# Kernel optimization log

Hardware: AMD Instinct MI355X
Metric: run time of the kernel (lower is better)

Reference implementation:

```python
import jax, jax.numpy as jnp
import numpy as np

H = 512        # hidden_size
ENC = 2 * H    # encoder (context) feature dim
V = 10000      # vocab_size
B, T, L = 32, 500, 100
NEG_INF = -1e10


def setup_inputs() -> dict:
    key = jax.random.key(0)
    ks = jax.random.split(key, 16)
    sc = 0.02
    inp = {
        "h_batch": jax.random.normal(ks[0], (B, T, ENC), jnp.float32),
        "seq_lens": jax.random.randint(ks[1], (B,), 1, T + 1),
        "labels": jax.random.randint(ks[2], (B, L), 0, V),
        # content-based (additive) attention params
        "attn_Ws": jax.random.normal(ks[3], (H, H), jnp.float32) * sc,
        "attn_Wh": jax.random.normal(ks[4], (ENC, H), jnp.float32) * sc,
        "attn_b": jnp.zeros((H,), jnp.float32),
        "attn_v": jax.random.normal(ks[5], (H,), jnp.float32) * sc,
        # output path
        "W_sy": jax.random.normal(ks[6], (H, H), jnp.float32) * sc,
        "b_sy": jnp.zeros((H,), jnp.float32),
        "W_gy": jax.random.normal(ks[7], (ENC, H), jnp.float32) * sc,
        "b_gy": jnp.zeros((H,), jnp.float32),
        "W_yy": jax.random.normal(ks[8], (H, V), jnp.float32) * sc,
        "b_yy": jnp.zeros((V,), jnp.float32),
        # recurrence path
        "E_yr": jax.random.normal(ks[9], (V, 4 * H), jnp.float32) * sc,
        "W_sr": jax.random.normal(ks[10], (H, 4 * H), jnp.float32) * sc,
        "b_sr": jnp.zeros((4 * H,), jnp.float32),
        "W_gr": jax.random.normal(ks[11], (ENC, 4 * H), jnp.float32) * sc,
        "b_gr": jnp.zeros((4 * H,), jnp.float32),
    }
    return inp


def _func_lstm(rec_in, c):
    i, f, g, o = jnp.split(rec_in, 4, axis=-1)
    c_new = jax.nn.sigmoid(f) * c + jax.nn.sigmoid(i) * jnp.tanh(g)
    s_new = jax.nn.sigmoid(o) * jnp.tanh(c_new)
    return s_new, c_new


def reference(h_batch, seq_lens, labels, attn_Ws, attn_Wh, attn_b, attn_v,
              W_sy, b_sy, W_gy, b_gy, W_yy, b_yy,
              E_yr, W_sr, b_sr, W_gr, b_gr):
    Tlen = h_batch.shape[1]
    mask = jnp.arange(Tlen)[None, :] < seq_lens[:, None]          # [B,T]
    h_proj = jnp.einsum('bte,eh->bth', h_batch, attn_Wh) + attn_b  # precompute

    s0 = jnp.zeros((h_batch.shape[0], H), h_batch.dtype)
    c0 = jnp.zeros_like(s0)

    def step(carry, y_t):
        s, c = carry
        # content-based attention: e = v . tanh(Ws s + Wh h)
        e = jnp.einsum('bth,h->bt', jnp.tanh(h_proj + (s @ attn_Ws)[:, None, :]), attn_v)
        e = jnp.where(mask, e, NEG_INF)
        alpha = jax.nn.softmax(e, axis=-1)                         # [B,T]
        g = jnp.einsum('bt,bte->be', alpha, h_batch)               # [B,ENC]
        dec_feat = (g @ W_gy + b_gy) + (s @ W_sy + b_sy)
        y = jnp.tanh(dec_feat) @ W_yy + b_yy                       # [B,V]
        rec_in = E_yr[y_t] + (s @ W_sr + b_sr) + (g @ W_gr + b_gr) # [B,4H]
        s_new, c_new = _func_lstm(rec_in, c)
        return (s_new, c_new), y

    _, preds = jax.lax.scan(step, (s0, c0), labels.T)              # [L,B,V]
    return jnp.transpose(preds, (1, 0, 2))                         # [B,L,V]
```

## Files before the change

kernel.cpp:

```cpp
#include <hip/hip_runtime.h>
#include <cstdint>

#define B_   32
#define T_   500
#define H_   512
#define ENC_ 1024
#define V_   10000
#define L_   100
#define H4_  2048
#define NB_  256
#define NT_  512

#define OFF_HPROJ 0
#define OFF_WYYP  4096000
#define OFF_WRECP 9216000
#define OFF_WSB   13148160
#define OFF_S     13279232
#define OFF_C0    13295616
#define OFF_C1    13312000
#define OFF_RACC  13328384
#define OFF_DACC  13393920
#define OFF_G0    13410304
#define OFF_G1    13443072
#define OFF_E     13475840
#define OFF_BAR   13492224
#define ZERO_CNT  213056

using bf16x8 = __attribute__((ext_vector_type(8))) short;
using f32x4  = __attribute__((ext_vector_type(4))) float;

__device__ __forceinline__ f32x4 mfma16(bf16x8 a, bf16x8 b, f32x4 c){
  return __builtin_amdgcn_mfma_f32_16x16x32_bf16(a, b, c, 0, 0, 0);
}
__device__ __forceinline__ unsigned short bfr(float f){
  unsigned x = __float_as_uint(f);
  return (unsigned short)((x + 0x7FFFu + ((x>>16)&1u)) >> 16);
}
__device__ __forceinline__ void bfsplit(float f, short& hi, short& lo){
  unsigned short h = bfr(f);
  float hf = __uint_as_float(((unsigned)h) << 16);
  hi = (short)h;
  lo = (short)bfr(f - hf);
}
__device__ __forceinline__ float bf2f(unsigned short u){
  return __uint_as_float(((unsigned)u) << 16);
}
__device__ __forceinline__ float ftanh(float x){
  float t = fminf(fmaxf(2.f*x, -30.f), 30.f);
  float e = __expf(t);
  return (e - 1.f) / (e + 1.f);
}
__device__ __forceinline__ float fsig(float x){
  float t = fminf(fmaxf(x, -30.f), 30.f);
  return 1.f / (1.f + __expf(-t));
}
__device__ __forceinline__ float gload(const float* p){
  return __hip_atomic_load((float*)p, __ATOMIC_RELAXED, __HIP_MEMORY_SCOPE_AGENT);
}
__device__ __forceinline__ void gstore(float* p, float v){
  __hip_atomic_store(p, v, __ATOMIC_RELAXED, __HIP_MEMORY_SCOPE_AGENT);
}
__device__ __forceinline__ void gload2(const float* p, float& a, float& b){
  unsigned long long u = __hip_atomic_load((const unsigned long long*)p,
                          __ATOMIC_RELAXED, __HIP_MEMORY_SCOPE_AGENT);
  a = __uint_as_float((unsigned)u);
  b = __uint_as_float((unsigned)(u >> 32));
}

__device__ __forceinline__ void gridbar(unsigned* bars, unsigned it){
  asm volatile("s_waitcnt vmcnt(0) lgkmcnt(0)" ::: "memory");
  __syncthreads();
  if (threadIdx.x == 0){
    unsigned* gc = bars + 1 + (blockIdx.x & 15);
    unsigned old = __hip_atomic_fetch_add(gc, 1u, __ATOMIC_RELAXED, __HIP_MEMORY_SCOPE_AGENT);
    if (old == it*16u + 15u)
      __hip_atomic_fetch_add(bars, 1u, __ATOMIC_RELAXED, __HIP_MEMORY_SCOPE_AGENT);
    while (__hip_atomic_load(bars, __ATOMIC_RELAXED, __HIP_MEMORY_SCOPE_AGENT) < (it+1u)*16u)
      __builtin_amdgcn_s_sleep(2);
  }
  __syncthreads();
  asm volatile("" ::: "memory");
}

__global__ void k_init(float* __restrict__ ws){
  int i = blockIdx.x * 256 + threadIdx.x;
  if (i < ZERO_CNT) ws[OFF_S + i] = 0.f;
}

__global__ void k_packWyy(const float* __restrict__ Wyy, float* __restrict__ ws){
  unsigned short* wp = (unsigned short*)(ws + OFF_WYYP);
  int t = blockIdx.x * 256 + threadIdx.x;
  if (t >= 625*16*64) return;
  int vt = t / 1024;
  int rem = t - vt*1024;
  int kc = rem >> 6, lane = rem & 63;
  int v  = vt*16 + (lane & 15);
  int k0 = kc*32 + ((lane >> 4) << 3);
  bf16x8 H, Lo;
  #pragma unroll
  for (int j = 0; j < 8; ++j){
    short h, lo; bfsplit(Wyy[(size_t)(k0+j)*V_ + v], h, lo);
    H[j] = h; Lo[j] = lo;
  }
  size_t base = ((size_t)(vt*16 + kc)*2)*512 + (size_t)lane*8;
  *(bf16x8*)(wp + base) = H;
  *(bf16x8*)(wp + base + 512) = Lo;
}

__global__ void k_packWrec(const float* __restrict__ Wsy, const float* __restrict__ Wgy,
                           const float* __restrict__ Wsr, const float* __restrict__ Wgr,
                           float* __restrict__ ws){
  unsigned short* wp = (unsigned short*)(ws + OFF_WRECP);
  int t = blockIdx.x * 256 + threadIdx.x;
  if (t >= 160*48*64) return;
  int vt = t / (48*64);
  int rem = t - vt*(48*64);
  int kc = rem >> 6, lane = rem & 63;
  int col = vt*16 + (lane & 15);
  int k0  = kc*32 + ((lane >> 4) << 3);
  bf16x8 H, Lo;
  #pragma unroll
  for (int j = 0; j < 8; ++j){
    int k = k0 + j;
    float x;
    if (k < 512) x = (col < 512) ? Wsy[(size_t)k*512 + col] : Wsr[(size_t)k*2048 + (col-512)];
    else         x = (col < 512) ? Wgy[(size_t)(k-512)*512 + col] : Wgr[(size_t)(k-512)*2048 + (col-512)];
    short h, lo; bfsplit(x, h, lo);
    H[j] = h; Lo[j] = lo;
  }
  size_t base = ((size_t)(vt*48 + kc)*2)*512 + (size_t)lane*8;
  *(bf16x8*)(wp + base) = H;
  *(bf16x8*)(wp + base + 512) = Lo;
}

__global__ void k_packWs(const float* __restrict__ Ws, float* __restrict__ ws){
  unsigned short* wp = (unsigned short*)(ws + OFF_WSB);
  int i = blockIdx.x * 256 + threadIdx.x;
  wp[i] = bfr(Ws[i]);
}

__global__ void k_hproj(const float* __restrict__ A, const float* __restrict__ W,
                        const float* __restrict__ bias, const int* __restrict__ lens,
                        float* __restrict__ ws){
  unsigned short* C = (unsigned short*)(ws + OFF_HPROJ);
  const int bm = blockIdx.x * 64;
  const int bn = blockIdx.y * 64;
  {
    int b0 = bm / T_, t0 = bm % T_;
    int b1 = (bm + 63) / T_;
    if (b0 == b1 && t0 >= lens[b0]) return;
  }
  __shared__ float As[64][33];
  __shared__ float Bs[32][68];
  const int tid = threadIdx.x;
  const int tx = tid & 15, ty = tid >> 4;
  float acc[4][4];
  #pragma unroll
  for (int i = 0; i < 4; ++i)
    #pragma unroll
    for (int j = 0; j < 4; ++j) acc[i][j] = 0.f;
  for (int k0 = 0; k0 < 1024; k0 += 32){
    for (int i = tid; i < 64*32; i += 256){
      int rr = i >> 5, cc = i & 31;
      As[rr][cc] = A[(size_t)(bm + rr) * 1024 + k0 + cc];
    }
    for (int i = tid; i < 32*64; i += 256){
      int rr = i >> 6, cc = i & 63;
      Bs[rr][cc] = W[(size_t)(k0 + rr) * 512 + bn + cc];
    }
    __syncthreads();
    #pragma unroll
    for (int kk = 0; kk < 32; ++kk){
      float a0 = As[ty*4+0][kk], a1 = As[ty*4+1][kk];
      float a2 = As[ty*4+2][kk], a3 = As[ty*4+3][kk];
      float4 b4 = *(const float4*)&Bs[kk][tx*4];
      acc[0][0] += a0*b4.x; acc[0][1] += a0*b4.y; acc[0][2] += a0*b4.z; acc[0][3] += a0*b4.w;
      acc[1][0] += a1*b4.x; acc[1][1] += a1*b4.y; acc[1][2] += a1*b4.z; acc[1][3] += a1*b4.w;
      acc[2][0] += a2*b4.x; acc[2][1] += a2*b4.y; acc[2][2] += a2*b4.z; acc[2][3] += a2*b4.w;
      acc[3][0] += a3*b4.x; acc[3][1] += a3*b4.y; acc[3][2] += a3*b4.z; acc[3][3] += a3*b4.w;
    }
    __syncthreads();
  }
  #pragma unroll
  for (int i = 0; i < 4; ++i){
    int m = bm + ty*4 + i;
    ushort4 o;
    o.x = bfr(acc[i][0] + bias[bn + tx*4 + 0]);
    o.y = bfr(acc[i][1] + bias[bn + tx*4 + 1]);
    o.z = bfr(acc[i][2] + bias[bn + tx*4 + 2]);
    o.w = bfr(acc[i][3] + bias[bn + tx*4 + 3]);
    *(ushort4*)&C[(size_t)m * 512 + bn + tx*4] = o;
  }
}

__global__ __launch_bounds__(NT_, 2) void k_persist(
    const float* __restrict__ hb,  const int* __restrict__ lens,
    const int* __restrict__ labels, const float* __restrict__ av,
    const float* __restrict__ bsy, const float* __restrict__ bgy,
    const float* __restrict__ byy,
    const float* __restrict__ Eyr,
    const float* __restrict__ bsr, const float* __restrict__ bgr,
    float* __restrict__ out, float* __restrict__ ws)
{
  const int blk = blockIdx.x;
  const int tid = threadIdx.x;
  const int w   = tid >> 6;
  const int lane= tid & 63;
  unsigned* bars = (unsigned*)(ws + OFF_BAR);
  const unsigned short* wyyp  = (const unsigned short*)(ws + OFF_WYYP);
  const unsigned short* wrecp = (const unsigned short*)(ws + OFF_WRECP);
  const unsigned short* wsb   = (const unsigned short*)(ws + OFF_WSB);
  const unsigned short* hpB   = (const unsigned short*)(ws + OFF_HPROJ);
  __shared__ __align__(16) float smem[4096];

  const int arow  = lane & 15;
  const int klane = (lane >> 4) << 3;
  float c_reg = 0.f;

  for (int l = 0; l <= L_; ++l){
    const int p = l & 1;
    const int goff = p ? OFF_G1 : OFF_G0;
    if (blk < 157){
      if (l > 0){
        const int kh = w & 1;
        const int vtslot = w >> 1;
        const int vt = blk*4 + vtslot;
        f32x4 a0 = {0.f,0.f,0.f,0.f}, a1 = {0.f,0.f,0.f,0.f};
        if (vt < 625){
          for (int kc2 = 0; kc2 < 8; ++kc2){
            const int kc = kh*8 + kc2;
            const int k0 = kc*32 + klane;
            float bb[8];
            {
              float4 y1 = *(const float4*)&bsy[k0];
              float4 y2 = *(const float4*)&bsy[k0+4];
              float4 y3 = *(const float4*)&bgy[k0];
              float4 y4 = *(const float4*)&bgy[k0+4];
              bb[0]=y1.x+y3.x; bb[1]=y1.y+y3.y; bb[2]=y1.z+y3.z; bb[3]=y1.w+y3.w;
              bb[4]=y2.x+y4.x; bb[5]=y2.y+y4.y; bb[6]=y2.z+y4.z; bb[7]=y2.w+y4.w;
            }
            bf16x8 Ahi0, Alo0, Ahi1, Alo1;
            {
              float x[8];
              gload2(&ws[OFF_DACC + arow*H_ + k0 + 0], x[0], x[1]);
              gload2(&ws[OFF_DACC + arow*H_ + k0 + 2], x[2], x[3]);
              gload2(&ws[OFF_DACC + arow*H_ + k0 + 4], x[4], x[5]);
              gload2(&ws[OFF_DACC + arow*H_ + k0 + 6], x[6], x[7]);
              #pragma unroll
              for (int j = 0; j < 8; ++j){
                short h, lo; bfsplit(ftanh(x[j] + bb[j]), h, lo);
                Ahi0[j] = h; Alo0[j] = lo;
              }
            }
            {
              float x[8];
              gload2(&ws[OFF_DACC + (arow+16)*H_ + k0 + 0], x[0], x[1]);
              gload2(&ws[OFF_DACC + (arow+16)*H_ + k0 + 2], x[2], x[3]);
              gload2(&ws[OFF_DACC + (arow+16)*H_ + k0 + 4], x[4], x[5]);
              gload2(&ws[OFF_DACC + (arow+16)*H_ + k0 + 6], x[6], x[7]);
              #pragma unroll
              for (int j = 0; j < 8; ++j){
                short h, lo; bfsplit(ftanh(x[j] + bb[j]), h, lo);
                Ahi1[j] = h; Alo1[j] = lo;
              }
            }
            const unsigned short* wp = wyyp + ((size_t)(vt*16 + kc)*2)*512 + (size_t)lane*8;
            bf16x8 Bhi = *(const bf16x8*)wp;
            bf16x8 Blo = *(const bf16x8*)(wp + 512);
            a0 = mfma16(Ahi0, Bhi, a0);
            a0 = mfma16(Alo0, Bhi, a0);
            a0 = mfma16(Ahi0, Blo, a0);
            a1 = mfma16(Ahi1, Bhi, a1);
            a1 = mfma16(Alo1, Bhi, a1);
            a1 = mfma16(Ahi1, Blo, a1);
          }
        }
        if (vt < 625 && kh == 0){
          #pragma unroll
          for (int r = 0; r < 4; ++r){
            smem[vtslot*512 +       lane*4 + r] = a0[r];
            smem[vtslot*512 + 256 + lane*4 + r] = a1[r];
          }
        }
        __syncthreads();
        if (vt < 625 && kh == 1){
          const int v = vt*16 + arow;
          const float bv = byy[v];
          const int lv = l - 1;
          #pragma unroll
          for (int r = 0; r < 4; ++r){
            const int row0 = ((lane >> 4) << 2) + r;
            float v0 = smem[vtslot*512 +       lane*4 + r] + a0[r] + bv;
            float v1 = smem[vtslot*512 + 256 + lane*4 + r] + a1[r] + bv;
            out[((size_t)(row0)*L_      + lv)*V_ + v] = v0;
            out[((size_t)(row0 + 16)*L_ + lv)*V_ + v] = v1;
          }
        }
        __syncthreads();
      }
    } else if (blk < 221){
      if (l < L_){
        const int u = blk - 157;
        const int b = u >> 1, half = u & 1;
        float* ssm = smem;
        float* part = smem + 512;
        float* wsm = smem + 2560;
        if (l == 0){
          ssm[tid] = 0.f;
          c_reg = 0.f;
        } else {
          const int h = tid;
          const float* ey = Eyr + (size_t)labels[b*L_ + (l-1)] * H4_;
          float ri = gload(&ws[OFF_RACC + b*H4_ + h])        + bsr[h]      + bgr[h]      + ey[h];
          float rf = gload(&ws[OFF_RACC + b*H4_ + 512 + h])  + bsr[512+h]  + bgr[512+h]  + ey[512+h];
          float rg = gload(&ws[OFF_RACC + b*H4_ + 1024 + h]) + bsr[1024+h] + bgr[1024+h] + ey[1024+h];
          float ro = gload(&ws[OFF_RACC + b*H4_ + 1536 + h]) + bsr[1536+h] + bgr[1536+h] + ey[1536+h];
          float cn = fsig(rf)*c_reg + fsig(ri)*ftanh(rg);
          float sn = fsig(ro)*ftanh(cn);
          c_reg = cn;
          if (half == 0) gstore(&ws[OFF_S + b*H_ + h], sn);
          ssm[h] = sn;
        }
        __syncthreads();
        {
          const int colp = tid & 255;
          const int kh2  = tid >> 8;
          const int col0 = colp*2;
          const float* sp = ssm + kh2*256;
          const unsigned short* wb = wsb + (size_t)(kh2*256)*512 + col0;
          float acc0 = 0.f, acc1 = 0.f;
          for (int k = 0; k < 256; k += 8){
            float4 s0 = *(const float4*)&sp[k];
            float4 s1 = *(const float4*)&sp[k+4];
            unsigned wv[8];
            #pragma unroll
            for (int j = 0; j < 8; ++j)
              wv[j] = *(const unsigned*)&wb[(size_t)(k+j)*512];
            float sv[8] = {s0.x,s0.y,s0.z,s0.w,s1.x,s1.y,s1.z,s1.w};
            #pragma unroll
            for (int j = 0; j < 8; ++j){
              acc0 += sv[j] * bf2f((unsigned short)(wv[j] & 0xFFFFu));
              acc1 += sv[j] * bf2f((unsigned short)(wv[j] >> 16));
            }
          }
          part[kh2*1024 + col0]     = acc0;
          part[kh2*1024 + col0 + 1] = acc1;
        }
        __syncthreads();
        wsm[tid] = part[tid] + part[1024 + tid];
        __syncthreads();
        const int len = lens[b];
        float avr[8], swr[8];
        #pragma unroll
        for (int j = 0; j < 8; ++j){
          avr[j] = av[lane*8 + j];
          swr[j] = wsm[lane*8 + j];
        }
        float* e = ws + OFF_E;
        for (int t = 2*w + half; t < len; t += 16){
          bf16x8 hp = *(const bf16x8*)&hpB[(size_t)(b*T_ + t)*512 + lane*8];
          float sum = 0.f;
          #pragma unroll
          for (int j = 0; j < 8; ++j)
            sum += avr[j] * ftanh(bf2f((unsigned short)hp[j]) + swr[j]);
          #pragma unroll
          for (int off = 32; off > 0; off >>= 1) sum += __shfl_xor(sum, off, 64);
          if (lane == 0) gstore(&e[b*T_ + t], sum);
        }
      }
    } else {
      if (l < L_){
        for (int i = (blk - 221)*NT_ + tid; i < B_*ENC_; i += 35*NT_)
          gstore(&ws[goff + i], 0.f);
      }
    }
    if (l == L_) break;
    gridbar(bars, (unsigned)(l*3 + 0));

    {
      const int b = blk >> 3, ts = blk & 7;
      const int len = lens[b];
      float* sc  = smem;
      float* red = smem + 512;
      float* pg  = smem + 1024;
      float val = (tid < len) ? gload(&ws[OFF_E + b*T_ + tid]) : -1e30f;
      sc[tid] = val;
      __syncthreads();
      if (tid < 256) red[tid] = fmaxf(sc[tid], sc[tid+256]);
      __syncthreads();
      for (int st = 128; st > 0; st >>= 1){
        if (tid < st) red[tid] = fmaxf(red[tid], red[tid+st]);
        __syncthreads();
      }
      const float mx = red[0];
      __syncthreads();
      float ex = (tid < len) ? __expf(val - mx) : 0.f;
      sc[tid] = ex;
      __syncthreads();
      if (tid < 256) red[tid] = sc[tid] + sc[tid+256];
      __syncthreads();
      for (int st = 128; st > 0; st >>= 1){
        if (tid < st) red[tid] += red[tid+st];
        __syncthreads();
      }
      const float inv = 1.f / red[0];
      const int tg  = tid >> 8;
      const int cq  = tid & 255;
      const int col = cq * 4;
      const float* hp = hb + (size_t)b*T_*ENC_ + col;
      float4 acc = {0.f,0.f,0.f,0.f};
      for (int t = ts*2 + tg; t < len; t += 16){
        float4 x = *(const float4*)&hp[(size_t)t * ENC_];
        float a = sc[t];
        acc.x += a*x.x; acc.y += a*x.y; acc.z += a*x.z; acc.w += a*x.w;
      }
      *(float4*)&pg[tg*1024 + col] = acc;
      __syncthreads();
      if (tid < 256){
        float4 x0 = *(const float4*)&pg[col];
        float4 x1 = *(const float4*)&pg[1024 + col];
        float* gp = ws + goff + b*ENC_ + col;
        atomicAdd(gp+0, (x0.x+x1.x)*inv);
        atomicAdd(gp+1, (x0.y+x1.y)*inv);
        atomicAdd(gp+2, (x0.z+x1.z)*inv);
        atomicAdd(gp+3, (x0.w+x1.w)*inv);
      }
    }
    gridbar(bars, (unsigned)(l*3 + 1));

    if (blk < 80){
      const int sub = w >> 2;
      const int w4  = w & 3;
      const int vt  = blk*2 + sub;
      f32x4 acc0 = {0.f,0.f,0.f,0.f}, acc1 = {0.f,0.f,0.f,0.f};
      for (int c = 0; c < 3; ++c){
        #pragma unroll
        for (int kc2 = 0; kc2 < 4; ++kc2){
          const int kc = c*16 + w4*4 + kc2;
          const int k0 = kc*32 + klane;
          bf16x8 Ahi0, Alo0, Ahi1, Alo1;
          {
            const float* src = (k0 < 512) ? &ws[OFF_S + arow*H_ + k0]
                                          : &ws[goff + arow*ENC_ + (k0 - 512)];
            float x[8];
            gload2(src+0, x[0], x[1]);
            gload2(src+2, x[2], x[3]);
            gload2(src+4, x[4], x[5]);
            gload2(src+6, x[6], x[7]);
            #pragma unroll
            for (int j = 0; j < 8; ++j){
              short h, lo; bfsplit(x[j], h, lo);
              Ahi0[j] = h; Alo0[j] = lo;
            }
          }
          {
            const float* src = (k0 < 512) ? &ws[OFF_S + (arow+16)*H_ + k0]
                                          : &ws[goff + (arow+16)*ENC_ + (k0 - 512)];
            float x[8];
            gload2(src+0, x[0], x[1]);
            gload2(src+2, x[2], x[3]);
            gload2(src+4, x[4], x[5]);
            gload2(src+6, x[6], x[7]);
            #pragma unroll
            for (int j = 0; j < 8; ++j){
              short h, lo; bfsplit(x[j], h, lo);
              Ahi1[j] = h; Alo1[j] = lo;
            }
          }
          const unsigned short* wp = wrecp + ((size_t)(vt*48 + kc)*2)*512 + (size_t)lane*8;
          bf16x8 Bhi = *(const bf16x8*)wp;
          bf16x8 Blo = *(const bf16x8*)(wp + 512);
          acc0 = mfma16(Ahi0, Bhi, acc0);
          acc0 = mfma16(Alo0, Bhi, acc0);
          acc0 = mfma16(Ahi0, Blo, acc0);
          acc1 = mfma16(Ahi1, Bhi, acc1);
          acc1 = mfma16(Alo1, Bhi, acc1);
          acc1 = mfma16(Ahi1, Blo, acc1);
        }
      }
      #pragma unroll
      for (int r = 0; r < 4; ++r){
        smem[sub*2048 + w4*512 +       lane*4 + r] = acc0[r];
        smem[sub*2048 + w4*512 + 256 + lane*4 + r] = acc1[r];
      }
      __syncthreads();
      #pragma unroll
      for (int oo = 0; oo < 2; ++oo){
        const int q   = tid + oo*512;
        const int sb  = q >> 9;
        const int rem = q & 511;
        const int bt  = rem >> 8;
        const int r8  = rem & 255;
        const int ln  = r8 >> 2, rr = r8 & 3;
        float v = smem[sb*2048 +        bt*256 + r8] + smem[sb*2048 +  512 + bt*256 + r8]
                + smem[sb*2048 + 1024 + bt*256 + r8] + smem[sb*2048 + 1536 + bt*256 + r8];
        const int row = bt*16 + ((ln >> 4) << 2) + rr;
        const int col = (blk*2 + sb)*16 + (ln & 15);
        if (col < 512) gstore(&ws[OFF_DACC + row*H_ + col], v);
        else           gstore(&ws[OFF_RACC + row*H4_ + (col - 512)], v);
      }
    }
    gridbar(bars, (unsigned)(l*3 + 2));
  }
}

extern "C" void kernel_launch(void* const* d_in, const int* in_sizes, int n_in,
                              void* d_out, int out_size, void* d_ws, size_t ws_size,
                              hipStream_t stream){
  const float* h_batch = (const float*)d_in[0];
  const int*   seq_lens= (const int*)d_in[1];
  const int*   labels  = (const int*)d_in[2];
  const float* attn_Ws = (const float*)d_in[3];
  const float* attn_Wh = (const float*)d_in[4];
  const float* attn_b  = (const float*)d_in[5];
  const float* attn_v  = (const float*)d_in[6];
  const float* W_sy    = (const float*)d_in[7];
  const float* b_sy    = (const float*)d_in[8];
  const float* W_gy    = (const float*)d_in[9];
  const float* b_gy    = (const float*)d_in[10];
  const float* W_yy    = (const float*)d_in[11];
  const float* b_yy    = (const float*)d_in[12];
  const float* E_yr    = (const float*)d_in[13];
  const float* W_sr    = (const float*)d_in[14];
  const float* b_sr    = (const float*)d_in[15];
  const float* W_gr    = (const float*)d_in[16];
  const float* b_gr    = (const float*)d_in[17];
  float* out = (float*)d_out;
  float* ws  = (float*)d_ws;

  k_init    <<<833, 256, 0, stream>>>(ws);
  k_packWyy <<<2500, 256, 0, stream>>>(W_yy, ws);
  k_packWrec<<<1920, 256, 0, stream>>>(W_sy, W_gy, W_sr, W_gr, ws);
  k_packWs  <<<1024, 256, 0, stream>>>(attn_Ws, ws);
  k_hproj   <<<dim3(250, 8), 256, 0, stream>>>(h_batch, attn_Wh, attn_b, seq_lens, ws);

  void* kargs[] = {
    (void*)&h_batch, (void*)&seq_lens, (void*)&labels, (void*)&attn_v,
    (void*)&b_sy, (void*)&b_gy, (void*)&b_yy,
    (void*)&E_yr, (void*)&b_sr, (void*)&b_gr,
    (void*)&out, (void*)&ws
  };
  hipLaunchCooperativeKernel((void*)k_persist, dim3(NB_), dim3(NT_), kargs, 0, stream);
}
```

Before: 10.82 ms.

## Use 1024-thread persistent blocks and bf16 copy of encoder states

Doubles the block size of the persistent cooperative kernel to 1024 threads with one block per CU. Work is redistributed so fewer blocks handle the vocab projection and recurrence GEMMs, and more waves handle attention scoring. A pre-pass converts h_batch to bf16 so the context-vector reduction reads half the bytes. Partial sums are now combined with shared-memory atomics, and the count of cross-block atomics on g drops. The trade-off is fewer resident waves per CU, an extra conversion kernel over 16M elements, and bf16 rounding of the encoder states in the context sum.

```diff
diff --git a/kernel.cpp b/kernel.cpp
--- a/kernel.cpp
+++ b/kernel.cpp
@@ -9,22 +9,21 @@
 #define L_   100
 #define H4_  2048
 #define NB_  256
-#define NT_  512
+#define NT_  1024
 
 #define OFF_HPROJ 0
 #define OFF_WYYP  4096000
 #define OFF_WRECP 9216000
 #define OFF_WSB   13148160
-#define OFF_S     13279232
-#define OFF_C0    13295616
-#define OFF_C1    13312000
-#define OFF_RACC  13328384
-#define OFF_DACC  13393920
-#define OFF_G0    13410304
-#define OFF_G1    13443072
-#define OFF_E     13475840
-#define OFF_BAR   13492224
-#define ZERO_CNT  213056
+#define OFF_HB16  13279232
+#define OFF_S     21471232
+#define OFF_RACC  21487616
+#define OFF_DACC  21553152
+#define OFF_G0    21569536
+#define OFF_G1    21602304
+#define OFF_E     21635072
+#define OFF_BAR   21651456
+#define ZERO_CNT  180288
 
 using bf16x8 = __attribute__((ext_vector_type(8))) short;
 using f32x4  = __attribute__((ext_vector_type(4))) float;
@@ -137,6 +136,12 @@
   unsigned short* wp = (unsigned short*)(ws + OFF_WSB);
   int i = blockIdx.x * 256 + threadIdx.x;
   wp[i] = bfr(Ws[i]);
+}
+
+__global__ void k_packHB(const float* __restrict__ hb, float* __restrict__ ws){
+  unsigned short* wp = (unsigned short*)(ws + OFF_HB16);
+  int i = blockIdx.x * 256 + threadIdx.x;
+  if (i < B_*T_*ENC_) wp[i] = bfr(hb[i]);
 }
 
 __global__ void k_hproj(const float* __restrict__ A, const float* __restrict__ W,
@@ -193,8 +198,8 @@
   }
 }
 
-__global__ __launch_bounds__(NT_, 2) void k_persist(
-    const float* __restrict__ hb,  const int* __restrict__ lens,
+__global__ __launch_bounds__(NT_, 1) void k_persist(
+    const int* __restrict__ lens,
     const int* __restrict__ labels, const float* __restrict__ av,
     const float* __restrict__ bsy, const float* __restrict__ bgy,
     const float* __restrict__ byy,
@@ -211,7 +216,8 @@
   const unsigned short* wrecp = (const unsigned short*)(ws + OFF_WRECP);
   const unsigned short* wsb   = (const unsigned short*)(ws + OFF_WSB);
   const unsigned short* hpB   = (const unsigned short*)(ws + OFF_HPROJ);
-  __shared__ __align__(16) float smem[4096];
+  const unsigned short* hb16  = (const unsigned short*)(ws + OFF_HB16);
+  __shared__ __align__(16) float smem[10240];
 
   const int arow  = lane & 15;
   const int klane = (lane >> 4) << 3;
@@ -220,13 +226,16 @@
   for (int l = 0; l <= L_; ++l){
     const int p = l & 1;
     const int goff = p ? OFF_G1 : OFF_G0;
-    if (blk < 157){
+    if (blk < 79){
       if (l > 0){
+        const int vtslot = w >> 1;
         const int kh = w & 1;
-        const int vtslot = w >> 1;
-        const int vt = blk*4 + vtslot;
-        f32x4 a0 = {0.f,0.f,0.f,0.f}, a1 = {0.f,0.f,0.f,0.f};
+        const int vt = blk*8 + vtslot;
+        float* cacc = smem;
+        for (int i = tid; i < 4096; i += NT_) cacc[i] = 0.f;
+        __syncthreads();
         if (vt < 625){
+          f32x4 a0 = {0.f,0.f,0.f,0.f}, a1 = {0.f,0.f,0.f,0.f};
           for (int kc2 = 0; kc2 < 8; ++kc2){
             const int kc = kh*8 + kc2;
             const int k0 = kc*32 + klane;
@@ -274,62 +283,60 @@
             a1 = mfma16(Alo1, Bhi, a1);
             a1 = mfma16(Ahi1, Blo, a1);
           }
-        }
-        if (vt < 625 && kh == 0){
           #pragma unroll
           for (int r = 0; r < 4; ++r){
-            smem[vtslot*512 +       lane*4 + r] = a0[r];
-            smem[vtslot*512 + 256 + lane*4 + r] = a1[r];
-          }
-        }
-        __syncthreads();
-        if (vt < 625 && kh == 1){
-          const int v = vt*16 + arow;
-          const float bv = byy[v];
-          const int lv = l - 1;
-          #pragma unroll
-          for (int r = 0; r < 4; ++r){
-            const int row0 = ((lane >> 4) << 2) + r;
-            float v0 = smem[vtslot*512 +       lane*4 + r] + a0[r] + bv;
-            float v1 = smem[vtslot*512 + 256 + lane*4 + r] + a1[r] + bv;
-            out[((size_t)(row0)*L_      + lv)*V_ + v] = v0;
-            out[((size_t)(row0 + 16)*L_ + lv)*V_ + v] = v1;
-          }
-        }
-        __syncthreads();
-      }
-    } else if (blk < 221){
+            atomicAdd(&cacc[vtslot*512 +       lane*4 + r], a0[r]);
+            atomicAdd(&cacc[vtslot*512 + 256 + lane*4 + r], a1[r]);
+          }
+        }
+        __syncthreads();
+        const int lv = l - 1;
+        #pragma unroll
+        for (int ii = 0; ii < 4; ++ii){
+          const int i = tid + ii*NT_;
+          const int vts = i >> 9, e9 = i & 511;
+          const int vto = blk*8 + vts;
+          if (vto < 625){
+            const int bt = e9 >> 8, r8 = e9 & 255, ln = r8 >> 2, rr = r8 & 3;
+            const int row = bt*16 + ((ln >> 4) << 2) + rr;
+            const int v = vto*16 + (ln & 15);
+            out[((size_t)row*L_ + lv)*V_ + v] = cacc[i] + byy[v];
+          }
+        }
+      }
+    } else if (blk < 207){
       if (l < L_){
-        const int u = blk - 157;
-        const int b = u >> 1, half = u & 1;
-        float* ssm = smem;
+        const int u = blk - 79;
+        const int b = u >> 2, q = u & 3;
+        float* ssm  = smem;
         float* part = smem + 512;
-        float* wsm = smem + 2560;
+        float* wsm  = smem + 2560;
         if (l == 0){
-          ssm[tid] = 0.f;
-          c_reg = 0.f;
+          if (tid < 512){ ssm[tid] = 0.f; c_reg = 0.f; }
         } else {
-          const int h = tid;
-          const float* ey = Eyr + (size_t)labels[b*L_ + (l-1)] * H4_;
-          float ri = gload(&ws[OFF_RACC + b*H4_ + h])        + bsr[h]      + bgr[h]      + ey[h];
-          float rf = gload(&ws[OFF_RACC + b*H4_ + 512 + h])  + bsr[512+h]  + bgr[512+h]  + ey[512+h];
-          float rg = gload(&ws[OFF_RACC + b*H4_ + 1024 + h]) + bsr[1024+h] + bgr[1024+h] + ey[1024+h];
-          float ro = gload(&ws[OFF_RACC + b*H4_ + 1536 + h]) + bsr[1536+h] + bgr[1536+h] + ey[1536+h];
-          float cn = fsig(rf)*c_reg + fsig(ri)*ftanh(rg);
-          float sn = fsig(ro)*ftanh(cn);
-          c_reg = cn;
-          if (half == 0) gstore(&ws[OFF_S + b*H_ + h], sn);
-          ssm[h] = sn;
+          if (tid < 512){
+            const int h = tid;
+            const float* ey = Eyr + (size_t)labels[b*L_ + (l-1)] * H4_;
+            float ri = gload(&ws[OFF_RACC + b*H4_ + h])        + bsr[h]      + bgr[h]      + ey[h];
+            float rf = gload(&ws[OFF_RACC + b*H4_ + 512 + h])  + bsr[512+h]  + bgr[512+h]  + ey[512+h];
+            float rg = gload(&ws[OFF_RACC + b*H4_ + 1024 + h]) + bsr[1024+h] + bgr[1024+h] + ey[1024+h];
+            float ro = gload(&ws[OFF_RACC + b*H4_ + 1536 + h]) + bsr[1536+h] + bgr[1536+h] + ey[1536+h];
+            float cn = fsig(rf)*c_reg + fsig(ri)*ftanh(rg);
+            float sn = fsig(ro)*ftanh(cn);
+            c_reg = cn;
+            if (q == 0) gstore(&ws[OFF_S + b*H_ + h], sn);
+            ssm[h] = sn;
+          }
         }
         __syncthreads();
         {
           const int colp = tid & 255;
-          const int kh2  = tid >> 8;
+          const int ksec = tid >> 8;
           const int col0 = colp*2;
-          const float* sp = ssm + kh2*256;
-          const unsigned short* wb = wsb + (size_t)(kh2*256)*512 + col0;
+          const float* sp = ssm + ksec*128;
+          const unsigned short* wb = wsb + (size_t)(ksec*128)*512 + col0;
           float acc0 = 0.f, acc1 = 0.f;
-          for (int k = 0; k < 256; k += 8){
+          for (int k = 0; k < 128; k += 8){
             float4 s0 = *(const float4*)&sp[k];
             float4 s1 = *(const float4*)&sp[k+4];
             unsigned wv[8];
@@ -343,11 +350,12 @@
               acc1 += sv[j] * bf2f((unsigned short)(wv[j] >> 16));
             }
           }
-          part[kh2*1024 + col0]     = acc0;
-          part[kh2*1024 + col0 + 1] = acc1;
-        }
-        __syncthreads();
-        wsm[tid] = part[tid] + part[1024 + tid];
+          part[ksec*512 + col0]     = acc0;
+          part[ksec*512 + col0 + 1] = acc1;
+        }
+        __syncthreads();
+        if (tid < 512)
+          wsm[tid] = part[tid] + part[512+tid] + part[1024+tid] + part[1536+tid];
         __syncthreads();
         const int len = lens[b];
         float avr[8], swr[8];
@@ -357,7 +365,7 @@
           swr[j] = wsm[lane*8 + j];
         }
         float* e = ws + OFF_E;
-        for (int t = 2*w + half; t < len; t += 16){
+        for (int t = w*4 + q; t < len; t += 64){
           bf16x8 hp = *(const bf16x8*)&hpB[(size_t)(b*T_ + t)*512 + lane*8];
           float sum = 0.f;
           #pragma unroll
@@ -368,9 +376,9 @@
           if (lane == 0) gstore(&e[b*T_ + t], sum);
         }
       }
-    } else {
+    } else if (blk < 223){
       if (l < L_){
-        for (int i = (blk - 221)*NT_ + tid; i < B_*ENC_; i += 35*NT_)
+        for (int i = (blk - 207)*NT_ + tid; i < B_*ENC_; i += 16*NT_)
           gstore(&ws[goff + i], 0.f);
       }
     }
@@ -383,8 +391,10 @@
       float* sc  = smem;
       float* red = smem + 512;
       float* pg  = smem + 1024;
-      float val = (tid < len) ? gload(&ws[OFF_E + b*T_ + tid]) : -1e30f;
-      sc[tid] = val;
+      if (tid < 512){
+        float val = (tid < len) ? gload(&ws[OFF_E + b*T_ + tid]) : -1e30f;
+        sc[tid] = val;
+      }
       __syncthreads();
       if (tid < 256) red[tid] = fmaxf(sc[tid], sc[tid+256]);
       __syncthreads();
@@ -394,8 +404,10 @@
       }
       const float mx = red[0];
       __syncthreads();
-      float ex = (tid < len) ? __expf(val - mx) : 0.f;
-      sc[tid] = ex;
+      if (tid < 512){
+        float ex = (tid < len) ? __expf(sc[tid] - mx) : 0.f;
+        sc[tid] = ex;
+      }
       __syncthreads();
       if (tid < 256) red[tid] = sc[tid] + sc[tid+256];
       __syncthreads();
@@ -404,96 +416,90 @@
         __syncthreads();
       }
       const float inv = 1.f / red[0];
-      const int tg  = tid >> 8;
-      const int cq  = tid & 255;
-      const int col = cq * 4;
-      const float* hp = hb + (size_t)b*T_*ENC_ + col;
-      float4 acc = {0.f,0.f,0.f,0.f};
-      for (int t = ts*2 + tg; t < len; t += 16){
-        float4 x = *(const float4*)&hp[(size_t)t * ENC_];
+      const int tg = tid >> 7;
+      const int cl = tid & 127;
+      const int col0 = cl*8;
+      const unsigned short* hp = hb16 + (size_t)b*T_*ENC_ + col0;
+      float acc[8] = {0.f,0.f,0.f,0.f,0.f,0.f,0.f,0.f};
+      for (int t = ts*8 + tg; t < len; t += 64){
+        bf16x8 x = *(const bf16x8*)&hp[(size_t)t * ENC_];
         float a = sc[t];
-        acc.x += a*x.x; acc.y += a*x.y; acc.z += a*x.z; acc.w += a*x.w;
-      }
-      *(float4*)&pg[tg*1024 + col] = acc;
-      __syncthreads();
-      if (tid < 256){
-        float4 x0 = *(const float4*)&pg[col];
-        float4 x1 = *(const float4*)&pg[1024 + col];
-        float* gp = ws + goff + b*ENC_ + col;
-        atomicAdd(gp+0, (x0.x+x1.x)*inv);
-        atomicAdd(gp+1, (x0.y+x1.y)*inv);
-        atomicAdd(gp+2, (x0.z+x1.z)*inv);
-        atomicAdd(gp+3, (x0.w+x1.w)*inv);
+        #pragma unroll
+        for (int j = 0; j < 8; ++j)
+          acc[j] += a * bf2f((unsigned short)x[j]);
+      }
+      *(float4*)&pg[tg*1024 + col0]     = *(float4*)&acc[0];
+      *(float4*)&pg[tg*1024 + col0 + 4] = *(float4*)&acc[4];
+      __syncthreads();
+      if (ts*8 < len){
+        float s = pg[tid] + pg[1024+tid] + pg[2048+tid] + pg[3072+tid]
+                + pg[4096+tid] + pg[5120+tid] + pg[6144+tid] + pg[7168+tid];
+        atomicAdd(&ws[goff + b*ENC_ + tid], s * inv);
       }
     }
     gridbar(bars, (unsigned)(l*3 + 1));
 
     if (blk < 80){
-      const int sub = w >> 2;
-      const int w4  = w & 3;
+      const int sub = w >> 3;
+      const int w8  = w & 7;
       const int vt  = blk*2 + sub;
+      float* cacc = smem;
+      for (int i = tid; i < 1024; i += NT_) cacc[i] = 0.f;
+      __syncthreads();
       f32x4 acc0 = {0.f,0.f,0.f,0.f}, acc1 = {0.f,0.f,0.f,0.f};
-      for (int c = 0; c < 3; ++c){
-        #pragma unroll
-        for (int kc2 = 0; kc2 < 4; ++kc2){
-          const int kc = c*16 + w4*4 + kc2;
-          const int k0 = kc*32 + klane;
-          bf16x8 Ahi0, Alo0, Ahi1, Alo1;
-          {
-            const float* src = (k0 < 512) ? &ws[OFF_S + arow*H_ + k0]
-                                          : &ws[goff + arow*ENC_ + (k0 - 512)];
-            float x[8];
-            gload2(src+0, x[0], x[1]);
-            gload2(src+2, x[2], x[3]);
-            gload2(src+4, x[4], x[5]);
-            gload2(src+6, x[6], x[7]);
-            #pragma unroll
-            for (int j = 0; j < 8; ++j){
-              short h, lo; bfsplit(x[j], h, lo);
-              Ahi0[j] = h; Alo0[j] = lo;
-            }
-          }
-          {
-            const float* src = (k0 < 512) ? &ws[OFF_S + (arow+16)*H_ + k0]
-                                          : &ws[goff + (arow+16)*ENC_ + (k0 - 512)];
-            float x[8];
-            gload2(src+0, x[0], x[1]);
-            gload2(src+2, x[2], x[3]);
-            gload2(src+4, x[4], x[5]);
-            gload2(src+6, x[6], x[7]);
-            #pragma unroll
-            for (int j = 0; j < 8; ++j){
-              short h, lo; bfsplit(x[j], h, lo);
-              Ahi1[j] = h; Alo1[j] = lo;
-            }
-          }
-          const unsigned short* wp = wrecp + ((size_t)(vt*48 + kc)*2)*512 + (size_t)lane*8;
-          bf16x8 Bhi = *(const bf16x8*)wp;
-          bf16x8 Blo = *(const bf16x8*)(wp + 512);
-          acc0 = mfma16(Ahi0, Bhi, acc0);
-          acc0 = mfma16(Alo0, Bhi, acc0);
-          acc0 = mfma16(Ahi0, Blo, acc0);
-          acc1 = mfma16(Ahi1, Bhi, acc1);
-          acc1 = mfma16(Alo1, Bhi, acc1);
-          acc1 = mfma16(Ahi1, Blo, acc1);
-        }
+      for (int j6 = 0; j6 < 6; ++j6){
+        const int kc = w8*6 + j6;
+        const int k0 = kc*32 + klane;
+        bf16x8 Ahi0, Alo0, Ahi1, Alo1;
+        {
+          const float* src = (k0 < 512) ? &ws[OFF_S + arow*H_ + k0]
+                                        : &ws[goff + arow*ENC_ + (k0 - 512)];
+          float x[8];
+          gload2(src+0, x[0], x[1]);
+          gload2(src+2, x[2], x[3]);
+          gload2(src+4, x[4], x[5]);
+          gload2(src+6, x[6], x[7]);
+          #pragma unroll
+          for (int j = 0; j < 8; ++j){
+            short h, lo; bfsplit(x[j], h, lo);
+            Ahi0[j] = h; Alo0[j] = lo;
+          }
+        }
+        {
+          const float* src = (k0 < 512) ? &ws[OFF_S + (arow+16)*H_ + k0]
+                                        : &ws[goff + (arow+16)*ENC_ + (k0 - 512)];
+          float x[8];
+          gload2(src+0, x[0], x[1]);
+          gload2(src+2, x[2], x[3]);
+          gload2(src+4, x[4], x[5]);
+          gload2(src+6, x[6], x[7]);
+          #pragma unroll
+          for (int j = 0; j < 8; ++j){
+            short h, lo; bfsplit(x[j], h, lo);
+            Ahi1[j] = h; Alo1[j] = lo;
+          }
+        }
+        const unsigned short* wp = wrecp + ((size_t)(vt*48 + kc)*2)*512 + (size_t)lane*8;
+        bf16x8 Bhi = *(const bf16x8*)wp;
+        bf16x8 Blo = *(const bf16x8*)(wp + 512);
+        acc0 = mfma16(Ahi0, Bhi, acc0);
+        acc0 = mfma16(Alo0, Bhi, acc0);
+        acc0 = mfma16(Ahi0, Blo, acc0);
+        acc1 = mfma16(Ahi1, Bhi, acc1);
+        acc1 = mfma16(Alo1, Bhi, acc1);
+        acc1 = mfma16(Ahi1, Blo, acc1);
       }
       #pragma unroll
       for (int r = 0; r < 4; ++r){
-        smem[sub*2048 + w4*512 +       lane*4 + r] = acc0[r];
-        smem[sub*2048 + w4*512 + 256 + lane*4 + r] = acc1[r];
-      }
-      __syncthreads();
-      #pragma unroll
-      for (int oo = 0; oo < 2; ++oo){
-        const int q   = tid + oo*512;
-        const int sb  = q >> 9;
-        const int rem = q & 511;
-        const int bt  = rem >> 8;
-        const int r8  = rem & 255;
-        const int ln  = r8 >> 2, rr = r8 & 3;
-        float v = smem[sb*2048 +        bt*256 + r8] + smem[sb*2048 +  512 + bt*256 + r8]
-                + smem[sb*2048 + 1024 + bt*256 + r8] + smem[sb*2048 + 1536 + bt*256 + r8];
+        atomicAdd(&cacc[sub*512 +       lane*4 + r], acc0[r]);
+        atomicAdd(&cacc[sub*512 + 256 + lane*4 + r], acc1[r]);
+      }
+      __syncthreads();
+      if (tid < 1024){
+        const int i = tid;
+        const int sb = i >> 9, e9 = i & 511;
+        const int bt = e9 >> 8, r8 = e9 & 255, ln = r8 >> 2, rr = r8 & 3;
+        const float v = cacc[i];
         const int row = bt*16 + ((ln >> 4) << 2) + rr;
         const int col = (blk*2 + sb)*16 + (ln & 15);
         if (col < 512) gstore(&ws[OFF_DACC + row*H_ + col], v);
@@ -528,14 +534,15 @@
   float* out = (float*)d_out;
   float* ws  = (float*)d_ws;
 
-  k_init    <<<833, 256, 0, stream>>>(ws);
+  k_init    <<<705, 256, 0, stream>>>(ws);
   k_packWyy <<<2500, 256, 0, stream>>>(W_yy, ws);
   k_packWrec<<<1920, 256, 0, stream>>>(W_sy, W_gy, W_sr, W_gr, ws);
   k_packWs  <<<1024, 256, 0, stream>>>(attn_Ws, ws);
+  k_packHB  <<<64000, 256, 0, stream>>>(h_batch, ws);
   k_hproj   <<<dim3(250, 8), 256, 0, stream>>>(h_batch, attn_Wh, attn_b, seq_lens, ws);
 
   void* kargs[] = {
-    (void*)&h_batch, (void*)&seq_lens, (void*)&labels, (void*)&attn_v,
+    (void*)&seq_lens, (void*)&labels, (void*)&attn_v,
     (void*)&b_sy, (void*)&b_gy, (void*)&b_yy,
     (void*)&E_yr, (void*)&b_sr, (void*)&b_gr,
     (void*)&out, (void*)&ws
```

Measured after the change: 16.41 ms. 1.52x slower.
